# Performance work log

Hardware: AMD Instinct MI355X
Metric: run time of the kernel (lower is better)

## Reference

```python
import jax, jax.numpy as jnp
import numpy as np

N, T, E = 20000, 4, 320000
IN_F, H_F, OUT_F, HEADS = 32, 16, 16, 8
NEG_SLOPE = 0.2


def gat_layer(x, W, al, ar, b, src, dst, n_nodes, heads, f_out):
    # x: [N, T, Fin], W: [Fin, heads*f_out], al/ar: [heads, f_out], b: [heads*f_out]
    feat = (x @ W).reshape(x.shape[0], x.shape[1], heads, f_out)      # [N,T,H,F]
    el = (feat * al).sum(-1)                                          # [N,T,H]
    er = (feat * ar).sum(-1)                                          # [N,T,H]
    e = jax.nn.leaky_relu(el[src] + er[dst], NEG_SLOPE)               # [E,T,H]
    # segment softmax over incoming edges of each destination node
    m = jax.lax.stop_gradient(jax.ops.segment_max(e, dst, num_segments=n_nodes))
    ex = jnp.exp(e - m[dst])
    s = jax.ops.segment_sum(ex, dst, num_segments=n_nodes)
    alpha = ex / s[dst]                                               # [E,T,H]
    msg = feat[src] * alpha[..., None]                                # [E,T,H,F]
    out = jax.ops.segment_sum(msg, dst, num_segments=n_nodes)
    return out + b.reshape(1, 1, heads, f_out)


def setup_inputs() -> dict:
    key = jax.random.key(0)
    ks = jax.random.split(key, 12)
    x = jax.random.normal(ks[0], (N, T, IN_F), dtype=jnp.float32)
    src = jax.random.randint(ks[1], (E,), 0, N)
    dst = jax.random.randint(ks[2], (E,), 0, N)
    s = 0.1
    W1 = jax.random.normal(ks[3], (IN_F, HEADS * H_F), dtype=jnp.float32) * s
    al1 = jax.random.normal(ks[4], (HEADS, H_F), dtype=jnp.float32) * s
    ar1 = jax.random.normal(ks[5], (HEADS, H_F), dtype=jnp.float32) * s
    b1 = jnp.zeros((HEADS * H_F,), dtype=jnp.float32)
    W2 = jax.random.normal(ks[6], (HEADS * H_F, OUT_F), dtype=jnp.float32) * s
    al2 = jax.random.normal(ks[7], (1, OUT_F), dtype=jnp.float32) * s
    ar2 = jax.random.normal(ks[8], (1, OUT_F), dtype=jnp.float32) * s
    b2 = jnp.zeros((OUT_F,), dtype=jnp.float32)
    return {"x": x, "src": src, "dst": dst, "W1": W1, "al1": al1, "ar1": ar1,
            "b1": b1, "W2": W2, "al2": al2, "ar2": ar2, "b2": b2}


def reference(x, src, dst, W1, al1, ar1, b1, W2, al2, ar2, b2):
    n = x.shape[0]
    h = gat_layer(x, W1, al1, ar1, b1, src, dst, n, HEADS, H_F)   # [N,T,H,F]
    h = h.reshape(n, h.shape[1], -1)                              # [N,T,H*F]
    h = gat_layer(h, W2, al2, ar2, b2, src, dst, n, 1, OUT_F)     # [N,T,1,OUT]
    return h.squeeze(2)                                           # [N,T,OUT]
```

## Files before the change

kernel.cpp:

```cpp
#include <hip/hip_runtime.h>
#include <hip/hip_fp16.h>
#include <math.h>

#define NN 20000
#define TT 4
#define EE 320000
#define NT (NN*TT)
#define H1 8
#define C1 128
#define IN_F 32
#define OUT_F 16
#define CAP 96
#define SCAT_BLOCKS 313
#define XCAST_BLOCKS 1250

typedef _Float16 h8 __attribute__((ext_vector_type(8)));
typedef float f32x4 __attribute__((ext_vector_type(4)));

__device__ __forceinline__ float lrelu_exp(float e) {
  e = (e >= 0.f) ? e : 0.2f * e;
  return __expf(e);
}

__global__ __launch_bounds__(256) void k_front(
    const float* __restrict__ x, const float* __restrict__ W1,
    const float* __restrict__ al1, const float* __restrict__ ar1,
    const float* __restrict__ W2, const float* __restrict__ al2,
    const float* __restrict__ ar2,
    const int4* __restrict__ src4, const int4* __restrict__ dst4,
    int* __restrict__ cnt, int* __restrict__ csr96,
    __half* __restrict__ xh, float* __restrict__ el1, float* __restrict__ er1,
    __half* __restrict__ W1hp, __half* __restrict__ W2pp) {
  __shared__ h8 ELERs[64];
  int b = blockIdx.x;
  int tid = threadIdx.x;
  if (b < SCAT_BLOCKS) {
    int e4 = b * 256 + tid;
    if (e4 < EE / 4) {
      int4 s = src4[e4];
      int4 d = dst4[e4];
      int p0 = atomicAdd(&cnt[d.x], 1); csr96[d.x * CAP + p0] = s.x;
      int p1 = atomicAdd(&cnt[d.y], 1); csr96[d.y * CAP + p1] = s.y;
      int p2 = atomicAdd(&cnt[d.z], 1); csr96[d.z * CAP + p2] = s.z;
      int p3 = atomicAdd(&cnt[d.w], 1); csr96[d.w * CAP + p3] = s.w;
    }
    return;
  }
  if (b == SCAT_BLOCKS) {
    for (int idx = tid; idx < 8 * 512; idx += 256) {
      int tile = idx >> 9;
      int rem = idx & 511;
      int lane = rem >> 3, j = rem & 7;
      int k = (lane >> 4) * 8 + j;
      int n = lane & 15;
      W1hp[idx] = __float2half(W1[k * C1 + tile * 16 + n]);
    }
    for (int idx = tid; idx < 8 * 512; idx += 256) {
      int tile = idx >> 9;
      int rem = idx & 511;
      int lane = rem >> 3, j = rem & 7;
      int ks = tile & 3;
      int k = ks * 32 + (lane >> 4) * 8 + j;
      int n = lane & 15;
      float v = 0.f;
      if (tile < 4) {
        v = W2[k * OUT_F + n];
      } else if (n == 0) {
        float s = 0.f;
        for (int f = 0; f < 16; ++f) s += W2[k * OUT_F + f] * al2[f];
        v = s;
      } else if (n == 1) {
        float s = 0.f;
        for (int f = 0; f < 16; ++f) s += W2[k * OUT_F + f] * ar2[f];
        v = s;
      }
      W2pp[idx] = __float2half(v);
    }
    return;
  }
  {
    __half* E = (__half*)ELERs;
    for (int idx = tid; idx < 512; idx += 256) {
      int lane = idx >> 3, j = idx & 7;
      int k = (lane >> 4) * 8 + j;
      int n = lane & 15;
      int hh_ = n & 7;
      const float* a = (n < 8) ? al1 : ar1;
      float s = 0.f;
      for (int f = 0; f < 16; ++f) s += W1[k * C1 + hh_ * 16 + f] * a[hh_ * 16 + f];
      E[idx] = __float2half(s);
    }
  }
  __syncthreads();
  int wave = tid >> 6, lane = tid & 63;
  int m = lane & 15, quad = lane >> 4;
  int rowbase = (b - SCAT_BLOCKS - 1) * 64 + wave * 16;
  int row = rowbase + m;
  const float4* xp = (const float4*)(x + row * IN_F + quad * 8);
  float4 a0 = xp[0], a1 = xp[1];
  h8 af;
  af[0] = (_Float16)a0.x; af[1] = (_Float16)a0.y;
  af[2] = (_Float16)a0.z; af[3] = (_Float16)a0.w;
  af[4] = (_Float16)a1.x; af[5] = (_Float16)a1.y;
  af[6] = (_Float16)a1.z; af[7] = (_Float16)a1.w;
  *(h8*)(xh + (size_t)row * IN_F + quad * 8) = af;
  {
    h8 bf = ELERs[lane];
    f32x4 c = {0.f, 0.f, 0.f, 0.f};
    c = __builtin_amdgcn_mfma_f32_16x16x32_f16(af, bf, c, 0, 0, 0);
#pragma unroll
    for (int r = 0; r < 4; ++r) {
      int orow = rowbase + quad * 4 + r;
      if (m < 8) el1[orow * H1 + m] = c[r];
      else       er1[orow * H1 + (m - 8)] = c[r];
    }
  }
}

__global__ __launch_bounds__(256, 4) void k_agg1m(
    const __half* __restrict__ xh,
    const float* __restrict__ el1,
    const float* __restrict__ er1,
    const int* __restrict__ cnt, const int* __restrict__ csr96,
    const __half* __restrict__ W1hp, const float* __restrict__ b1,
    const __half* __restrict__ W2pp,
    __half* __restrict__ feat2h, float* __restrict__ el2,
    float* __restrict__ er2) {
  __shared__ __half axs[16][264];
  __shared__ __half hs[16][136];
  int tid = threadIdx.x;
  int wv = tid >> 6, lane = tid & 63;
  int n = blockIdx.x * 4 + wv;
  int slot = lane >> 1;
  int t = lane >> 4;
  int hf = lane & 1;
  float er_i = er1[(size_t)n * 32 + slot];
  int deg = cnt[n];
  const int* eb = csr96 + (size_t)n * CAP;
  h8 accA = {0, 0, 0, 0, 0, 0, 0, 0};
  h8 accB = {0, 0, 0, 0, 0, 0, 0, 0};
  float l = 0.f;
  for (int chunk = 0; chunk < deg; chunk += 64) {
    int m = min(64, deg - chunk);
    int sv = (lane < m) ? eb[chunk + lane] : 0;
    int iters = (m + 3) >> 2;
    for (int g = 0; g < iters; ++g) {
      int j = g * 4;
      int s0 = __builtin_amdgcn_readlane(sv, j + 0);
      int s1 = __builtin_amdgcn_readlane(sv, j + 1);
      int s2 = __builtin_amdgcn_readlane(sv, j + 2);
      int s3 = __builtin_amdgcn_readlane(sv, j + 3);
      float ew0 = el1[(size_t)s0 * 32 + slot];
      float ew1 = el1[(size_t)s1 * 32 + slot];
      float ew2 = el1[(size_t)s2 * 32 + slot];
      float ew3 = el1[(size_t)s3 * 32 + slot];
      const __half* x0 = xh + (size_t)(s0 * 4 + t) * 32 + hf * 16;
      const __half* x1 = xh + (size_t)(s1 * 4 + t) * 32 + hf * 16;
      const __half* x2 = xh + (size_t)(s2 * 4 + t) * 32 + hf * 16;
      const __half* x3 = xh + (size_t)(s3 * 4 + t) * 32 + hf * 16;
      h8 a0 = *(const h8*)x0, b0 = *(const h8*)(x0 + 8);
      h8 a1 = *(const h8*)x1, b1_ = *(const h8*)(x1 + 8);
      h8 a2 = *(const h8*)x2, b2_ = *(const h8*)(x2 + 8);
      h8 a3 = *(const h8*)x3, b3_ = *(const h8*)(x3 + 8);
#define CONSUME(K, EW, XA, XB)                                    \
      {                                                           \
        float w_ = lrelu_exp(EW + er_i);                          \
        w_ = (j + K < m) ? w_ : 0.f;                              \
        l += w_;                                                  \
        _Float16 wh_ = (_Float16)w_;                              \
        h8 w8_ = {wh_, wh_, wh_, wh_, wh_, wh_, wh_, wh_};        \
        accA += w8_ * XA;                                         \
        accB += w8_ * XB;                                         \
      }
      CONSUME(0, ew0, a0, b0) CONSUME(1, ew1, a1, b1_)
      CONSUME(2, ew2, a2, b2_) CONSUME(3, ew3, a3, b3_)
#undef CONSUME
    }
  }
  float inv = (l > 0.f) ? (1.f / l) : 0.f;
  {
    h8 r0, r1;
#pragma unroll
    for (int q = 0; q < 8; ++q) {
      r0[q] = (_Float16)((float)accA[q] * inv);
      r1[q] = (_Float16)((float)accB[q] * inv);
    }
    int hh_ = slot & 7;
    __half* op = &axs[wv * 4 + t][hh_ * 32 + hf * 16];
    *(h8*)op = r0;
    *(h8*)(op + 8) = r1;
  }
  __syncthreads();

  int m = lane & 15, quad = lane >> 4;
  const h8* bp1 = (const h8*)W1hp;
#pragma unroll
  for (int hi = 0; hi < 2; ++hi) {
    int head = wv * 2 + hi;
    h8 af = *(const h8*)&axs[m][head * 32 + quad * 8];
    f32x4 c = {0.f, 0.f, 0.f, 0.f};
    c = __builtin_amdgcn_mfma_f32_16x16x32_f16(af, bp1[head * 64 + lane], c, 0, 0, 0);
    float bv = b1[head * 16 + m];
#pragma unroll
    for (int r = 0; r < 4; ++r)
      hs[quad * 4 + r][head * 16 + m] = __float2half(c[r] + bv);
  }
  __syncthreads();
  if (wv != 0) return;
  const h8* bp2 = (const h8*)W2pp;
  f32x4 cF = {0.f, 0.f, 0.f, 0.f};
  f32x4 cE = {0.f, 0.f, 0.f, 0.f};
#pragma unroll
  for (int ks = 0; ks < 4; ++ks) {
    h8 af = *(const h8*)&hs[m][ks * 32 + quad * 8];
    cF = __builtin_amdgcn_mfma_f32_16x16x32_f16(af, bp2[ks * 64 + lane], cF, 0, 0, 0);
    cE = __builtin_amdgcn_mfma_f32_16x16x32_f16(af, bp2[(4 + ks) * 64 + lane], cE, 0, 0, 0);
  }
#pragma unroll
  for (int r = 0; r < 4; ++r) {
    int orow = blockIdx.x * 16 + quad * 4 + r;
    feat2h[(size_t)orow * OUT_F + m] = __float2half(cF[r]);
    if (m == 0) el2[orow] = cE[r];
    if (m == 1) er2[orow] = cE[r];
  }
}

__global__ __launch_bounds__(256, 4) void k_agg2x(
    const __half* __restrict__ feat2h,
    const float* __restrict__ el2, const float* __restrict__ er2,
    const int* __restrict__ cnt, const int* __restrict__ csr96,
    const float* __restrict__ b2, float* __restrict__ out) {
  int tid = threadIdx.x;
  int wv = tid >> 6, lane = tid & 63;
  int n = blockIdx.x * 4 + wv;
  int t = lane >> 4, f = lane & 15;
  float ern = er2[n * 4 + t];
  int deg = cnt[n];
  const int* eb = csr96 + (size_t)n * CAP;
  float acc = 0.f, l = 0.f;
  for (int chunk = 0; chunk < deg; chunk += 64) {
    int m = min(64, deg - chunk);
    int sv = (lane < m) ? eb[chunk + lane] : 0;
    int iters = (m + 7) >> 3;
    for (int g = 0; g < iters; ++g) {
      int j = g * 8;
      int s0 = __builtin_amdgcn_readlane(sv, j + 0);
      int s1 = __builtin_amdgcn_readlane(sv, j + 1);
      int s2 = __builtin_amdgcn_readlane(sv, j + 2);
      int s3 = __builtin_amdgcn_readlane(sv, j + 3);
      int s4 = __builtin_amdgcn_readlane(sv, j + 4);
      int s5 = __builtin_amdgcn_readlane(sv, j + 5);
      int s6 = __builtin_amdgcn_readlane(sv, j + 6);
      int s7 = __builtin_amdgcn_readlane(sv, j + 7);
      float e0 = el2[s0 * 4 + t];
      float e1 = el2[s1 * 4 + t];
      float e2 = el2[s2 * 4 + t];
      float e3 = el2[s3 * 4 + t];
      float e4 = el2[s4 * 4 + t];
      float e5 = el2[s5 * 4 + t];
      float e6 = el2[s6 * 4 + t];
      float e7 = el2[s7 * 4 + t];
      __half f0 = feat2h[(size_t)(s0 * 4 + t) * OUT_F + f];
      __half f1 = feat2h[(size_t)(s1 * 4 + t) * OUT_F + f];
      __half f2 = feat2h[(size_t)(s2 * 4 + t) * OUT_F + f];
      __half f3 = feat2h[(size_t)(s3 * 4 + t) * OUT_F + f];
      __half f4 = feat2h[(size_t)(s4 * 4 + t) * OUT_F + f];
      __half f5 = feat2h[(size_t)(s5 * 4 + t) * OUT_F + f];
      __half f6 = feat2h[(size_t)(s6 * 4 + t) * OUT_F + f];
      __half f7 = feat2h[(size_t)(s7 * 4 + t) * OUT_F + f];
#define CONSUME(K, EW, FV)                                        \
      {                                                           \
        float w_ = lrelu_exp(EW + ern);                           \
        w_ = (j + K < m) ? w_ : 0.f;                              \
        l += w_;                                                  \
        acc = fmaf(w_, __half2float(FV), acc);                    \
      }
      CONSUME(0, e0, f0) CONSUME(1, e1, f1)
      CONSUME(2, e2, f2) CONSUME(3, e3, f3)
      CONSUME(4, e4, f4) CONSUME(5, e5, f5)
      CONSUME(6, e6, f6) CONSUME(7, e7, f7)
#undef CONSUME
    }
  }
  float inv = (l > 0.f) ? (1.f / l) : 0.f;
  out[(size_t)(n * 4 + t) * OUT_F + f] = acc * inv + b2[f];
}

extern "C" void kernel_launch(void* const* d_in, const int* in_sizes, int n_in,
                              void* d_out, int out_size, void* d_ws, size_t ws_size,
                              hipStream_t stream) {
  const float* x   = (const float*)d_in[0];
  const int*   src = (const int*)d_in[1];
  const int*   dst = (const int*)d_in[2];
  const float* W1  = (const float*)d_in[3];
  const float* al1 = (const float*)d_in[4];
  const float* ar1 = (const float*)d_in[5];
  const float* b1  = (const float*)d_in[6];
  const float* W2  = (const float*)d_in[7];
  const float* al2 = (const float*)d_in[8];
  const float* ar2 = (const float*)d_in[9];
  const float* b2  = (const float*)d_in[10];
  float* out = (float*)d_out;

  char* w = (char*)d_ws;
  __half* xh     = (__half*)w; w += (size_t)NT * IN_F * 2;
  __half* feat2h = (__half*)w; w += (size_t)NT * OUT_F * 2;
  float*  el1    = (float*)w;  w += (size_t)NT * H1 * 4;
  float*  er1    = (float*)w;  w += (size_t)NT * H1 * 4;
  float*  el2    = (float*)w;  w += (size_t)NT * 4;
  float*  er2    = (float*)w;  w += (size_t)NT * 4;
  __half* W1hp   = (__half*)w; w += (size_t)8 * 512 * 2;
  __half* W2pp   = (__half*)w; w += (size_t)8 * 512 * 2;
  int* cnt     = (int*)w;      w += (size_t)NN * 4;
  int* csr96   = (int*)w;      w += (size_t)NN * CAP * 4;

  hipMemsetAsync(cnt, 0, NN * sizeof(int), stream);

  k_front<<<SCAT_BLOCKS + 1 + XCAST_BLOCKS, 256, 0, stream>>>(
      x, W1, al1, ar1, W2, al2, ar2, (const int4*)src, (const int4*)dst,
      cnt, csr96, xh, el1, er1, W1hp, W2pp);
  k_agg1m<<<NN / 4, 256, 0, stream>>>(xh, el1, er1, cnt, csr96,
                                      W1hp, b1, W2pp, feat2h, el2, er2);
  k_agg2x<<<NN / 4, 256, 0, stream>>>(feat2h, el2, er2, cnt, csr96, b2, out);
}
```

Baseline: 150.5 us.

## Stage gathered neighbor rows through LDS with cooperative 16-byte loads in aggregation kernels

Both aggregation kernels now gather 16 neighbors' el and feature rows per step. Lanes are spread across 16-byte segments of those rows, fetched with full-width vector loads, written to a per-wave LDS staging buffer, then read back per lane for the weighted accumulation. This replaces per-lane narrow gathers (scalar floats and halves repeated across lanes) with fewer, wider and coalesced global loads. The cost is extra LDS traffic and footprint, bpermute index shuffles, and padded work on partial chunks. Occupancy may drop from the added shared memory, and no explicit barrier is placed between the per-wave LDS write and read.

```diff
diff --git a/kernel.cpp b/kernel.cpp
--- a/kernel.cpp
+++ b/kernel.cpp
@@ -126,6 +126,7 @@
     const __half* __restrict__ W2pp,
     __half* __restrict__ feat2h, float* __restrict__ el2,
     float* __restrict__ er2) {
+  __shared__ int4 stg4[4][384];
   __shared__ __half axs[16][264];
   __shared__ __half hs[16][136];
   int tid = threadIdx.x;
@@ -137,44 +138,47 @@
   float er_i = er1[(size_t)n * 32 + slot];
   int deg = cnt[n];
   const int* eb = csr96 + (size_t)n * CAP;
+  const char* el1b = (const char*)el1;
+  const char* xhb  = (const char*)xh;
+  char* myst = (char*)stg4[wv];
   h8 accA = {0, 0, 0, 0, 0, 0, 0, 0};
   h8 accB = {0, 0, 0, 0, 0, 0, 0, 0};
   float l = 0.f;
   for (int chunk = 0; chunk < deg; chunk += 64) {
-    int m = min(64, deg - chunk);
-    int sv = (lane < m) ? eb[chunk + lane] : 0;
-    int iters = (m + 3) >> 2;
-    for (int g = 0; g < iters; ++g) {
-      int j = g * 4;
-      int s0 = __builtin_amdgcn_readlane(sv, j + 0);
-      int s1 = __builtin_amdgcn_readlane(sv, j + 1);
-      int s2 = __builtin_amdgcn_readlane(sv, j + 2);
-      int s3 = __builtin_amdgcn_readlane(sv, j + 3);
-      float ew0 = el1[(size_t)s0 * 32 + slot];
-      float ew1 = el1[(size_t)s1 * 32 + slot];
-      float ew2 = el1[(size_t)s2 * 32 + slot];
-      float ew3 = el1[(size_t)s3 * 32 + slot];
-      const __half* x0 = xh + (size_t)(s0 * 4 + t) * 32 + hf * 16;
-      const __half* x1 = xh + (size_t)(s1 * 4 + t) * 32 + hf * 16;
-      const __half* x2 = xh + (size_t)(s2 * 4 + t) * 32 + hf * 16;
-      const __half* x3 = xh + (size_t)(s3 * 4 + t) * 32 + hf * 16;
-      h8 a0 = *(const h8*)x0, b0 = *(const h8*)(x0 + 8);
-      h8 a1 = *(const h8*)x1, b1_ = *(const h8*)(x1 + 8);
-      h8 a2 = *(const h8*)x2, b2_ = *(const h8*)(x2 + 8);
-      h8 a3 = *(const h8*)x3, b3_ = *(const h8*)(x3 + 8);
-#define CONSUME(K, EW, XA, XB)                                    \
-      {                                                           \
-        float w_ = lrelu_exp(EW + er_i);                          \
-        w_ = (j + K < m) ? w_ : 0.f;                              \
-        l += w_;                                                  \
-        _Float16 wh_ = (_Float16)w_;                              \
-        h8 w8_ = {wh_, wh_, wh_, wh_, wh_, wh_, wh_, wh_};        \
-        accA += w8_ * XA;                                         \
-        accB += w8_ * XB;                                         \
-      }
-      CONSUME(0, ew0, a0, b0) CONSUME(1, ew1, a1, b1_)
-      CONSUME(2, ew2, a2, b2_) CONSUME(3, ew3, a3, b3_)
-#undef CONSUME
+    int m64 = min(64, deg - chunk);
+    int sv = (lane < m64) ? eb[chunk + lane] : 0;
+    int nq = (m64 + 15) >> 4;
+    for (int q = 0; q < nq; ++q) {
+      int mc = min(16, m64 - q * 16);
+      int4 st[6];
+#pragma unroll
+      for (int i = 0; i < 6; ++i) {
+        int g = i * 64 + lane;
+        int e = g / 24;
+        int seg = g - e * 24;
+        int ec = (e < mc) ? e : (mc - 1);
+        int s = __builtin_amdgcn_ds_bpermute(((q << 4) + ec) << 2, sv);
+        const char* p = (seg < 8)
+            ? (el1b + (size_t)s * 128 + seg * 16)
+            : (xhb  + (size_t)s * 256 + (seg - 8) * 16);
+        st[i] = *(const int4*)p;
+      }
+#pragma unroll
+      for (int i = 0; i < 6; ++i)
+        *(int4*)(myst + i * 1024 + lane * 16) = st[i];
+#pragma unroll
+      for (int e = 0; e < 16; ++e) {
+        float ew = *(const float*)(myst + e * 384 + slot * 4);
+        h8 xa = *(const h8*)(myst + e * 384 + 128 + t * 64 + hf * 32);
+        h8 xb = *(const h8*)(myst + e * 384 + 128 + t * 64 + hf * 32 + 16);
+        float w_ = lrelu_exp(ew + er_i);
+        w_ = (e < mc) ? w_ : 0.f;
+        l += w_;
+        _Float16 wh_ = (_Float16)w_;
+        h8 w8_ = {wh_, wh_, wh_, wh_, wh_, wh_, wh_, wh_};
+        accA += w8_ * xa;
+        accB += w8_ * xb;
+      }
     }
   }
   float inv = (l > 0.f) ? (1.f / l) : 0.f;
@@ -230,6 +234,7 @@
     const float* __restrict__ el2, const float* __restrict__ er2,
     const int* __restrict__ cnt, const int* __restrict__ csr96,
     const float* __restrict__ b2, float* __restrict__ out) {
+  __shared__ int4 stg4[4][192];
   int tid = threadIdx.x;
   int wv = tid >> 6, lane = tid & 63;
   int n = blockIdx.x * 4 + wv;
@@ -237,49 +242,42 @@
   float ern = er2[n * 4 + t];
   int deg = cnt[n];
   const int* eb = csr96 + (size_t)n * CAP;
+  const char* f2b = (const char*)feat2h;
+  const char* e2b = (const char*)el2;
+  char* myst = (char*)stg4[wv];
   float acc = 0.f, l = 0.f;
   for (int chunk = 0; chunk < deg; chunk += 64) {
-    int m = min(64, deg - chunk);
-    int sv = (lane < m) ? eb[chunk + lane] : 0;
-    int iters = (m + 7) >> 3;
-    for (int g = 0; g < iters; ++g) {
-      int j = g * 8;
-      int s0 = __builtin_amdgcn_readlane(sv, j + 0);
-      int s1 = __builtin_amdgcn_readlane(sv, j + 1);
-      int s2 = __builtin_amdgcn_readlane(sv, j + 2);
-      int s3 = __builtin_amdgcn_readlane(sv, j + 3);
-      int s4 = __builtin_amdgcn_readlane(sv, j + 4);
-      int s5 = __builtin_amdgcn_readlane(sv, j + 5);
-      int s6 = __builtin_amdgcn_readlane(sv, j + 6);
-      int s7 = __builtin_amdgcn_readlane(sv, j + 7);
-      float e0 = el2[s0 * 4 + t];
-      float e1 = el2[s1 * 4 + t];
-      float e2 = el2[s2 * 4 + t];
-      float e3 = el2[s3 * 4 + t];
-      float e4 = el2[s4 * 4 + t];
-      float e5 = el2[s5 * 4 + t];
-      float e6 = el2[s6 * 4 + t];
-      float e7 = el2[s7 * 4 + t];
-      __half f0 = feat2h[(size_t)(s0 * 4 + t) * OUT_F + f];
-      __half f1 = feat2h[(size_t)(s1 * 4 + t) * OUT_F + f];
-      __half f2 = feat2h[(size_t)(s2 * 4 + t) * OUT_F + f];
-      __half f3 = feat2h[(size_t)(s3 * 4 + t) * OUT_F + f];
-      __half f4 = feat2h[(size_t)(s4 * 4 + t) * OUT_F + f];
-      __half f5 = feat2h[(size_t)(s5 * 4 + t) * OUT_F + f];
-      __half f6 = feat2h[(size_t)(s6 * 4 + t) * OUT_F + f];
-      __half f7 = feat2h[(size_t)(s7 * 4 + t) * OUT_F + f];
-#define CONSUME(K, EW, FV)                                        \
-      {                                                           \
-        float w_ = lrelu_exp(EW + ern);                           \
-        w_ = (j + K < m) ? w_ : 0.f;                              \
-        l += w_;                                                  \
-        acc = fmaf(w_, __half2float(FV), acc);                    \
-      }
-      CONSUME(0, e0, f0) CONSUME(1, e1, f1)
-      CONSUME(2, e2, f2) CONSUME(3, e3, f3)
-      CONSUME(4, e4, f4) CONSUME(5, e5, f5)
-      CONSUME(6, e6, f6) CONSUME(7, e7, f7)
-#undef CONSUME
+    int m64 = min(64, deg - chunk);
+    int sv = (lane < m64) ? eb[chunk + lane] : 0;
+    int nq = (m64 + 15) >> 4;
+    for (int q = 0; q < nq; ++q) {
+      int mc = min(16, m64 - q * 16);
+      int4 st[3];
+#pragma unroll
+      for (int i = 0; i < 3; ++i) {
+        int g = i * 64 + lane;
+        int e = g / 9;
+        int seg = g - e * 9;
+        if (e > 15) { e = 15; seg = 8; }
+        int ec = (e < mc) ? e : (mc - 1);
+        int s = __builtin_amdgcn_ds_bpermute(((q << 4) + ec) << 2, sv);
+        const char* p = (seg < 8)
+            ? (f2b + (size_t)s * 128 + seg * 16)
+            : (e2b + (size_t)s * 16);
+        st[i] = *(const int4*)p;
+      }
+#pragma unroll
+      for (int i = 0; i < 3; ++i)
+        *(int4*)(myst + i * 1024 + lane * 16) = st[i];
+#pragma unroll
+      for (int e = 0; e < 16; ++e) {
+        float ew = *(const float*)(myst + e * 144 + 128 + t * 4);
+        __half fv = *(const __half*)(myst + e * 144 + t * 32 + f * 2);
+        float w_ = lrelu_exp(ew + ern);
+        w_ = (e < mc) ? w_ : 0.f;
+        l += w_;
+        acc = fmaf(w_, __half2float(fv), acc);
+      }
     }
   }
   float inv = (l > 0.f) ? (1.f / l) : 0.f;
```

New measurement: 168.9 us. 1.12x slower.

## Stage gathered neighbor rows through LDS with coalesced 16-byte loads in agg1

Applied to the files above, without the earlier changes.

The layer-1 aggregation now gathers 16 neighbors at a time. Each lane loads 16-byte segments of the el1 row (128B) and the xh row (256B) chosen via ds_bpermute, writes them to a per-wave LDS staging buffer, and the weighted accumulation then reads from LDS. This replaces the scattered per-lane 4-byte and 16-byte global loads with fewer, full-width coalesced loads issued in one batch for more memory-level parallelism. It costs 24KB of extra LDS per block, which may reduce occupancy. The launch-bounds occupancy hint on k_agg2x is also removed.

```diff
diff --git a/kernel.cpp b/kernel.cpp
--- a/kernel.cpp
+++ b/kernel.cpp
@@ -126,6 +126,7 @@
     const __half* __restrict__ W2pp,
     __half* __restrict__ feat2h, float* __restrict__ el2,
     float* __restrict__ er2) {
+  __shared__ int4 stg4[4][384];
   __shared__ __half axs[16][264];
   __shared__ __half hs[16][136];
   int tid = threadIdx.x;
@@ -137,44 +138,47 @@
   float er_i = er1[(size_t)n * 32 + slot];
   int deg = cnt[n];
   const int* eb = csr96 + (size_t)n * CAP;
+  const char* el1b = (const char*)el1;
+  const char* xhb  = (const char*)xh;
+  char* myst = (char*)stg4[wv];
   h8 accA = {0, 0, 0, 0, 0, 0, 0, 0};
   h8 accB = {0, 0, 0, 0, 0, 0, 0, 0};
   float l = 0.f;
   for (int chunk = 0; chunk < deg; chunk += 64) {
-    int m = min(64, deg - chunk);
-    int sv = (lane < m) ? eb[chunk + lane] : 0;
-    int iters = (m + 3) >> 2;
-    for (int g = 0; g < iters; ++g) {
-      int j = g * 4;
-      int s0 = __builtin_amdgcn_readlane(sv, j + 0);
-      int s1 = __builtin_amdgcn_readlane(sv, j + 1);
-      int s2 = __builtin_amdgcn_readlane(sv, j + 2);
-      int s3 = __builtin_amdgcn_readlane(sv, j + 3);
-      float ew0 = el1[(size_t)s0 * 32 + slot];
-      float ew1 = el1[(size_t)s1 * 32 + slot];
-      float ew2 = el1[(size_t)s2 * 32 + slot];
-      float ew3 = el1[(size_t)s3 * 32 + slot];
-      const __half* x0 = xh + (size_t)(s0 * 4 + t) * 32 + hf * 16;
-      const __half* x1 = xh + (size_t)(s1 * 4 + t) * 32 + hf * 16;
-      const __half* x2 = xh + (size_t)(s2 * 4 + t) * 32 + hf * 16;
-      const __half* x3 = xh + (size_t)(s3 * 4 + t) * 32 + hf * 16;
-      h8 a0 = *(const h8*)x0, b0 = *(const h8*)(x0 + 8);
-      h8 a1 = *(const h8*)x1, b1_ = *(const h8*)(x1 + 8);
-      h8 a2 = *(const h8*)x2, b2_ = *(const h8*)(x2 + 8);
-      h8 a3 = *(const h8*)x3, b3_ = *(const h8*)(x3 + 8);
-#define CONSUME(K, EW, XA, XB)                                    \
-      {                                                           \
-        float w_ = lrelu_exp(EW + er_i);                          \
-        w_ = (j + K < m) ? w_ : 0.f;                              \
-        l += w_;                                                  \
-        _Float16 wh_ = (_Float16)w_;                              \
-        h8 w8_ = {wh_, wh_, wh_, wh_, wh_, wh_, wh_, wh_};        \
-        accA += w8_ * XA;                                         \
-        accB += w8_ * XB;                                         \
+    int m64 = min(64, deg - chunk);
+    int sv = (lane < m64) ? eb[chunk + lane] : 0;
+    int nq = (m64 + 15) >> 4;
+    for (int q = 0; q < nq; ++q) {
+      int mc = min(16, m64 - q * 16);
+      int4 st[6];
+#pragma unroll
+      for (int i = 0; i < 6; ++i) {
+        int g = i * 64 + lane;
+        int e = g / 24;
+        int seg = g - e * 24;
+        int ec = (e < mc) ? e : (mc - 1);
+        int s = __builtin_amdgcn_ds_bpermute(((q << 4) + ec) << 2, sv);
+        const char* p = (seg < 8)
+            ? (el1b + (size_t)s * 128 + seg * 16)
+            : (xhb  + (size_t)s * 256 + (seg - 8) * 16);
+        st[i] = *(const int4*)p;
       }
-      CONSUME(0, ew0, a0, b0) CONSUME(1, ew1, a1, b1_)
-      CONSUME(2, ew2, a2, b2_) CONSUME(3, ew3, a3, b3_)
-#undef CONSUME
+#pragma unroll
+      for (int i = 0; i < 6; ++i)
+        *(int4*)(myst + i * 1024 + lane * 16) = st[i];
+#pragma unroll
+      for (int e = 0; e < 16; ++e) {
+        float ew = *(const float*)(myst + e * 384 + slot * 4);
+        h8 xa = *(const h8*)(myst + e * 384 + 128 + t * 64 + hf * 32);
+        h8 xb = *(const h8*)(myst + e * 384 + 128 + t * 64 + hf * 32 + 16);
+        float w_ = lrelu_exp(ew + er_i);
+        w_ = (e < mc) ? w_ : 0.f;
+        l += w_;
+        _Float16 wh_ = (_Float16)w_;
+        h8 w8_ = {wh_, wh_, wh_, wh_, wh_, wh_, wh_, wh_};
+        accA += w8_ * xa;
+        accB += w8_ * xb;
+      }
     }
   }
   float inv = (l > 0.f) ? (1.f / l) : 0.f;
@@ -225,7 +229,7 @@
   }
 }
 
-__global__ __launch_bounds__(256, 4) void k_agg2x(
+__global__ __launch_bounds__(256) void k_agg2x(
     const __half* __restrict__ feat2h,
     const float* __restrict__ el2, const float* __restrict__ er2,
     const int* __restrict__ cnt, const int* __restrict__ csr96,
```

New measurement: 166.1 us. +10.4%, slower.
